# Kernel optimization log

Hardware: AMD Instinct MI355X
Metric: run time of the kernel (lower is better)

Reference implementation:

```python
import jax, jax.numpy as jnp
import numpy as np

N, E, H, C, NG = 50000, 800000, 4, 64, 32
HC = H * C  # 256


def setup_inputs() -> dict:
    key = jax.random.key(0)
    ks = jax.random.split(key, 32)
    f32 = jnp.float32
    def rn(k, shape, s=0.1):
        return jax.random.normal(k, shape, dtype=f32) * s
    inp = {}
    inp['x'] = jax.random.normal(ks[0], (N, 4), dtype=f32)
    inp['edge_index'] = jax.random.randint(ks[1], (2, E), 0, N, dtype=jnp.int32)
    inp['edge_attr'] = jax.random.normal(ks[2], (E, 1), dtype=f32)
    inp['batch'] = jnp.sort(jax.random.randint(ks[3], (N,), 0, NG, dtype=jnp.int32))
    # encoder
    inp['enc_w'] = rn(ks[4], (4, 64)); inp['enc_b'] = rn(ks[5], (64,))
    # GATv2 layer 1: in 64 -> H*C (lin_l source, lin_r target, lin_edge, att, bias)
    inp['g1_wl'] = rn(ks[6], (64, HC)); inp['g1_bl'] = rn(ks[7], (HC,))
    inp['g1_wr'] = rn(ks[8], (64, HC)); inp['g1_br'] = rn(ks[9], (HC,))
    inp['g1_we'] = rn(ks[10], (1, HC))
    inp['g1_att'] = rn(ks[11], (H, C))
    inp['g1_bias'] = rn(ks[12], (HC,))
    # GATv2 layer 2: in 256 -> H*C
    inp['g2_wl'] = rn(ks[13], (HC, HC)); inp['g2_bl'] = rn(ks[14], (HC,))
    inp['g2_wr'] = rn(ks[15], (HC, HC)); inp['g2_br'] = rn(ks[16], (HC,))
    inp['g2_we'] = rn(ks[17], (1, HC))
    inp['g2_att'] = rn(ks[18], (H, C))
    inp['g2_bias'] = rn(ks[19], (HC,))
    # post MLP: 256 -> 128 (LayerNorm, ReLU) -> 64 (ReLU)
    inp['p1_w'] = rn(ks[20], (HC, 128)); inp['p1_b'] = rn(ks[21], (128,))
    inp['ln_g'] = jnp.ones((128,), dtype=f32); inp['ln_b'] = jnp.zeros((128,), dtype=f32)
    inp['p2_w'] = rn(ks[22], (128, 64)); inp['p2_b'] = rn(ks[23], (64,))
    return inp


def _gatv2_layer(x, src, dst, eattr, wl, bl, wr, br, we, att, bias):
    # PyG GATv2Conv: alpha_e = att . leaky_relu(lin_l(x_src) + lin_r(x_dst) + lin_edge(e))
    n = x.shape[0]
    xl = (x @ wl + bl).reshape(n, H, C)   # source-side messages
    xr = (x @ wr + br).reshape(n, H, C)   # target-side
    e = (eattr @ we).reshape(-1, H, C)
    m = jax.nn.leaky_relu(xl[src] + xr[dst] + e, 0.2)        # [E',H,C]
    alpha = jnp.einsum('ehc,hc->eh', m, att)                  # [E',H]
    amax = jax.lax.stop_gradient(jax.ops.segment_max(alpha, dst, num_segments=n))
    ex = jnp.exp(alpha - amax[dst])
    den = jax.ops.segment_sum(ex, dst, num_segments=n)
    a = ex / den[dst]                                          # softmax per dst node
    out = jax.ops.segment_sum(a[:, :, None] * xl[src], dst, num_segments=n)
    return out.reshape(n, HC) + bias


def reference(x, edge_index, edge_attr, batch, enc_w, enc_b,
              g1_wl, g1_bl, g1_wr, g1_br, g1_we, g1_att, g1_bias,
              g2_wl, g2_bl, g2_wr, g2_br, g2_we, g2_att, g2_bias,
              p1_w, p1_b, ln_g, ln_b, p2_w, p2_b):
    n = x.shape[0]
    src0, dst0 = edge_index[0], edge_index[1]
    # PyG default add_self_loops=True with fill_value='mean' for edge_attr
    deg = jnp.maximum(jax.ops.segment_sum(jnp.ones_like(edge_attr[:, 0]), dst0, num_segments=n), 1.0)
    loop_attr = jax.ops.segment_sum(edge_attr, dst0, num_segments=n) / deg[:, None]
    idx = jnp.arange(n, dtype=src0.dtype)
    src = jnp.concatenate([src0, idx]); dst = jnp.concatenate([dst0, idx])
    eattr = jnp.concatenate([edge_attr, loop_attr], axis=0)
    h = jax.nn.relu(x @ enc_w + enc_b)
    h = jax.nn.relu(_gatv2_layer(h, src, dst, eattr, g1_wl, g1_bl, g1_wr, g1_br, g1_we, g1_att, g1_bias))
    h = jax.nn.relu(_gatv2_layer(h, src, dst, eattr, g2_wl, g2_bl, g2_wr, g2_br, g2_we, g2_att, g2_bias))
    # global mean pool over graphs
    cnt = jnp.maximum(jax.ops.segment_sum(jnp.ones((n,), h.dtype), batch, num_segments=NG), 1.0)
    g = jax.ops.segment_sum(h, batch, num_segments=NG) / cnt[:, None]
    # post MLP (dropout is identity in eval)
    z = g @ p1_w + p1_b
    mu = jnp.mean(z, axis=-1, keepdims=True)
    var = jnp.mean((z - mu) ** 2, axis=-1, keepdims=True)
    z = (z - mu) / jnp.sqrt(var + 1e-5) * ln_g + ln_b
    z = jax.nn.relu(z)
    z = jax.nn.relu(z @ p2_w + p2_b)
    return z
```

## Files before the change

### kernel.cpp

```cpp
#include <hip/hip_runtime.h>

#define CDIV(a,b) (((a)+(b)-1)/(b))

typedef __bf16 bf16_t;
typedef bf16_t bf16x8 __attribute__((ext_vector_type(8)));
typedef bf16_t bf16x4 __attribute__((ext_vector_type(4)));
typedef float floatx4 __attribute__((ext_vector_type(4)));
typedef float floatx2 __attribute__((ext_vector_type(2)));

__device__ __forceinline__ int sigma2(int p) {
    int tile = p >> 7, hh = (p >> 6) & 1, m = (p >> 2) & 15, c = p & 3;
    return tile * 128 + (hh * 4 + c) * 16 + m;
}

__device__ __forceinline__ floatx2 up2(unsigned v) {
    floatx2 r;
    r.x = __uint_as_float(v << 16);
    r.y = __uint_as_float(v & 0xffff0000u);
    return r;
}

__global__ void k_deg(const int* __restrict__ ei, const float* __restrict__ ea,
                      int* __restrict__ deg, float* __restrict__ lsum, int E) {
    int e = blockIdx.x * 256 + threadIdx.x;
    if (e >= E) return;
    int d = ei[E + e];
    atomicAdd(&deg[d], 1);
    atomicAdd(&lsum[d], ea[e]);
}

__global__ void k_scanA(const int* __restrict__ deg, int* __restrict__ part, int n) {
    __shared__ int sh[256];
    int t = threadIdx.x;
    int i = blockIdx.x * 256 + t;
    int v = (i < n) ? deg[i] + 1 : 0;
    sh[t] = v;
    __syncthreads();
    for (int d = 128; d > 0; d >>= 1) { if (t < d) sh[t] += sh[t + d]; __syncthreads(); }
    if (t == 0) part[blockIdx.x] = sh[0];
}
__global__ void k_scanB(int* __restrict__ part, int nb) {
    __shared__ int sh[256];
    int t = threadIdx.x;
    int v = (t < nb) ? part[t] : 0;
    sh[t] = v;
    __syncthreads();
    for (int d = 1; d < 256; d <<= 1) {
        int u = (t >= d) ? sh[t - d] : 0;
        __syncthreads();
        sh[t] += u;
        __syncthreads();
    }
    if (t < nb) part[t] = sh[t] - v;
}
__global__ void k_scanC(const int* __restrict__ deg, const int* __restrict__ part,
                        int* __restrict__ off, float* __restrict__ lsum, int n) {
    __shared__ int sh[256];
    int t = threadIdx.x;
    int i = blockIdx.x * 256 + t;
    int dv = (i < n) ? deg[i] : 0;
    int v = (i < n) ? dv + 1 : 0;
    sh[t] = v;
    __syncthreads();
    for (int d = 1; d < 256; d <<= 1) {
        int u = (t >= d) ? sh[t - d] : 0;
        __syncthreads();
        sh[t] += u;
        __syncthreads();
    }
    int excl = part[blockIdx.x] + sh[t] - v;
    if (i < n) {
        off[i] = excl;
        lsum[i] = lsum[i] / fmaxf((float)dv, 1.0f);
    }
    if (i == n - 1) off[n] = excl + v;
}

__global__ void k_fill(const int* __restrict__ ei, const float* __restrict__ ea,
                       const float* __restrict__ lattr, const int* __restrict__ off,
                       int* __restrict__ cursor, int2* __restrict__ csr, int E, int n) {
    int e = blockIdx.x * 256 + threadIdx.x;
    int EE = E + n;
    if (e >= EE) return;
    int s, d; float a;
    if (e < E) { s = ei[e]; d = ei[E + e]; a = ea[e]; }
    else       { s = e - E; d = s;         a = lattr[s]; }
    int pos = off[d] + atomicAdd(&cursor[d], 1);
    csr[pos] = make_int2(s, __float_as_int(a));
}

__global__ void k_wcast2(const float* __restrict__ Wl, const float* __restrict__ Wr,
                         const float* __restrict__ bl, const float* __restrict__ br,
                         bf16_t* __restrict__ Wt, float* __restrict__ bias2,
                         int K, int kshift, int permK,
                         const float* __restrict__ we, const float* __restrict__ att,
                         const float* __restrict__ cb,
                         float* __restrict__ wep, float* __restrict__ attp,
                         float* __restrict__ cbp) {
    int idx = blockIdx.x * 256 + threadIdx.x;
    if (idx < 512) bias2[idx] = (idx < 256) ? bl[idx] : br[idx - 256];
    if (idx < 256) {
        int sg = sigma2(idx);
        wep[idx] = we[sg]; attp[idx] = att[sg]; cbp[idx] = cb[sg];
    }
    if (idx >= 512 * K) return;
    int nn = idx >> kshift, k = idx & (K - 1);
    int ks = permK ? sigma2(k) : k;
    float v = (nn < 256) ? Wl[ks * 256 + nn] : Wr[ks * 256 + (nn - 256)];
    Wt[idx] = (bf16_t)v;
}

__global__ __launch_bounds__(256) void k_gemm1_fused(
        const float* __restrict__ x, const float* __restrict__ encw,
        const float* __restrict__ encb, const bf16_t* __restrict__ Wt,
        const float* __restrict__ bias2, bf16_t* __restrict__ XL,
        bf16_t* __restrict__ XR, int nrows) {
    __shared__ bf16_t As[128 * 32];
    __shared__ bf16_t Bs[128 * 32];
    int tid = threadIdx.x;
    int w = tid >> 6, lane = tid & 63;
    int quad = lane >> 4, m = lane & 15;
    int row0 = blockIdx.x * 128;
    int n0 = blockIdx.y * 128;
    floatx4 acc[2][8];
#pragma unroll
    for (int rt = 0; rt < 2; ++rt)
#pragma unroll
        for (int ct = 0; ct < 8; ++ct)
            acc[rt][ct] = (floatx4){0.f, 0.f, 0.f, 0.f};

    for (int k0 = 0; k0 < 64; k0 += 32) {
        __syncthreads();
#pragma unroll
        for (int i = 0; i < 2; ++i) {
            int c = tid + i * 256;
            int r = c >> 2, kc = c & 3;
            int sw = (kc + (r >> 1)) & 3;
            int gr = row0 + r; if (gr >= nrows) gr = nrows - 1;
            float4 xv = ((const float4*)x)[gr];
            bf16x8 v;
#pragma unroll
            for (int kk = 0; kk < 8; ++kk) {
                int k = k0 + kc * 8 + kk;
                float s = encb[k];
                s = fmaf(xv.x, encw[k], s);
                s = fmaf(xv.y, encw[64 + k], s);
                s = fmaf(xv.z, encw[128 + k], s);
                s = fmaf(xv.w, encw[192 + k], s);
                v[kk] = (bf16_t)fmaxf(s, 0.0f);
            }
            *(bf16x8*)&As[r * 32 + sw * 8] = v;
        }
#pragma unroll
        for (int i = 0; i < 2; ++i) {
            int c = tid + i * 256;
            int r = c >> 2, kc = c & 3;
            int sw = (kc + (r >> 1)) & 3;
            bf16x8 v = *(const bf16x8*)&Wt[(size_t)(n0 + r) * 64 + k0 + kc * 8];
            *(bf16x8*)&Bs[r * 32 + sw * 8] = v;
        }
        __syncthreads();
        bf16x8 af[2], bfr[8];
#pragma unroll
        for (int rt = 0; rt < 2; ++rt) {
            int ar = w * 32 + rt * 16 + m;
            af[rt] = *(bf16x8*)&As[ar * 32 + (((quad + (ar >> 1)) & 3) * 8)];
        }
#pragma unroll
        for (int ct = 0; ct < 8; ++ct) {
            int br = ct * 16 + m;
            bfr[ct] = *(bf16x8*)&Bs[br * 32 + (((quad + (br >> 1)) & 3) * 8)];
        }
#pragma unroll
        for (int ct = 0; ct < 8; ++ct) {
            acc[0][ct] = __builtin_amdgcn_mfma_f32_16x16x32_bf16(af[0], bfr[ct], acc[0][ct], 0, 0, 0);
            acc[1][ct] = __builtin_amdgcn_mfma_f32_16x16x32_bf16(af[1], bfr[ct], acc[1][ct], 0, 0, 0);
        }
    }
    int tile = (n0 >> 7) & 1;
    bf16_t* dst = (n0 < 256) ? XL : XR;
    float bv[8];
#pragma unroll
    for (int ct = 0; ct < 8; ++ct) bv[ct] = bias2[n0 + ct * 16 + m];
#pragma unroll
    for (int rt = 0; rt < 2; ++rt) {
#pragma unroll
        for (int i = 0; i < 4; ++i) {
            int row = row0 + w * 32 + rt * 16 + quad * 4 + i;
            if (row < nrows) {
                bf16x4 v0, v1;
#pragma unroll
                for (int ct = 0; ct < 4; ++ct) {
                    v0[ct] = (bf16_t)(acc[rt][ct][i] + bv[ct]);
                    v1[ct] = (bf16_t)(acc[rt][ct + 4][i] + bv[ct + 4]);
                }
                *(bf16x4*)&dst[(size_t)row * 256 + tile * 128 + m * 4] = v0;
                *(bf16x4*)&dst[(size_t)row * 256 + tile * 128 + 64 + m * 4] = v1;
            }
        }
    }
}

__global__ __launch_bounds__(256) void k_gemm_mfma(
        const bf16_t* __restrict__ Hb, const bf16_t* __restrict__ Wt,
        const float* __restrict__ bias2, bf16_t* __restrict__ XL,
        bf16_t* __restrict__ XR, int nrows, int K) {
    __shared__ bf16_t As[128 * 32];
    __shared__ bf16_t Bs[128 * 32];
    int tid = threadIdx.x;
    int w = tid >> 6, lane = tid & 63;
    int quad = lane >> 4, m = lane & 15;
    int row0 = blockIdx.x * 128;
    int n0 = blockIdx.y * 128;
    floatx4 acc[2][8];
#pragma unroll
    for (int rt = 0; rt < 2; ++rt)
#pragma unroll
        for (int ct = 0; ct < 8; ++ct)
            acc[rt][ct] = (floatx4){0.f, 0.f, 0.f, 0.f};

    for (int k0 = 0; k0 < K; k0 += 32) {
        __syncthreads();
#pragma unroll
        for (int i = 0; i < 2; ++i) {
            int c = tid + i * 256;
            int r = c >> 2, kc = c & 3;
            int sw = (kc + (r >> 1)) & 3;
            int gr = row0 + r; if (gr >= nrows) gr = nrows - 1;
            bf16x8 v = *(const bf16x8*)&Hb[(size_t)gr * K + k0 + kc * 8];
            *(bf16x8*)&As[r * 32 + sw * 8] = v;
        }
#pragma unroll
        for (int i = 0; i < 2; ++i) {
            int c = tid + i * 256;
            int r = c >> 2, kc = c & 3;
            int sw = (kc + (r >> 1)) & 3;
            bf16x8 v = *(const bf16x8*)&Wt[(size_t)(n0 + r) * K + k0 + kc * 8];
            *(bf16x8*)&Bs[r * 32 + sw * 8] = v;
        }
        __syncthreads();
        bf16x8 af[2], bfr[8];
#pragma unroll
        for (int rt = 0; rt < 2; ++rt) {
            int ar = w * 32 + rt * 16 + m;
            af[rt] = *(bf16x8*)&As[ar * 32 + (((quad + (ar >> 1)) & 3) * 8)];
        }
#pragma unroll
        for (int ct = 0; ct < 8; ++ct) {
            int br = ct * 16 + m;
            bfr[ct] = *(bf16x8*)&Bs[br * 32 + (((quad + (br >> 1)) & 3) * 8)];
        }
#pragma unroll
        for (int ct = 0; ct < 8; ++ct) {
            acc[0][ct] = __builtin_amdgcn_mfma_f32_16x16x32_bf16(af[0], bfr[ct], acc[0][ct], 0, 0, 0);
            acc[1][ct] = __builtin_amdgcn_mfma_f32_16x16x32_bf16(af[1], bfr[ct], acc[1][ct], 0, 0, 0);
        }
    }
    int tile = (n0 >> 7) & 1;
    bf16_t* dst = (n0 < 256) ? XL : XR;
    float bv[8];
#pragma unroll
    for (int ct = 0; ct < 8; ++ct) bv[ct] = bias2[n0 + ct * 16 + m];
#pragma unroll
    for (int rt = 0; rt < 2; ++rt) {
#pragma unroll
        for (int i = 0; i < 4; ++i) {
            int row = row0 + w * 32 + rt * 16 + quad * 4 + i;
            if (row < nrows) {
                bf16x4 v0, v1;
#pragma unroll
                for (int ct = 0; ct < 4; ++ct) {
                    v0[ct] = (bf16_t)(acc[rt][ct][i] + bv[ct]);
                    v1[ct] = (bf16_t)(acc[rt][ct + 4][i] + bv[ct + 4]);
                }
                *(bf16x4*)&dst[(size_t)row * 256 + tile * 128 + m * 4] = v0;
                *(bf16x4*)&dst[(size_t)row * 256 + tile * 128 + 64 + m * 4] = v1;
            }
        }
    }
}

__device__ __forceinline__ void pair_step(
        int p, int p1, int half, int loff,
        const int2* __restrict__ csr, const bf16_t* __restrict__ XL,
        floatx2 xr01, floatx2 xr23, floatx2 xr45, floatx2 xr67,
        floatx2 wv01, floatx2 wv23, floatx2 wv45, floatx2 wv67,
        floatx2 av01, floatx2 av23, floatx2 av45, floatx2 av67,
        float& s, floatx2& a01, floatx2& a23, floatx2& a45, floatx2& a67) {
    int idx = p + half;
    bool valid = idx < p1;
    int idc = valid ? idx : p1 - 1;
    int2 ed = csr[idc];
    int src = ed.x;
    float eav = __int_as_float(ed.y);
    uint4 u = *(const uint4*)((const char*)XL + (size_t)src * 512 + loff);
    floatx2 x01 = up2(u.x), x23 = up2(u.y), x45 = up2(u.z), x67 = up2(u.w);
    floatx2 t01 = x01 + xr01 + eav * wv01;
    floatx2 t23 = x23 + xr23 + eav * wv23;
    floatx2 t45 = x45 + xr45 + eav * wv45;
    floatx2 t67 = x67 + xr67 + eav * wv67;
    t01 = __builtin_elementwise_max(t01, 0.2f * t01);
    t23 = __builtin_elementwise_max(t23, 0.2f * t23);
    t45 = __builtin_elementwise_max(t45, 0.2f * t45);
    t67 = __builtin_elementwise_max(t67, 0.2f * t67);
    floatx2 d = t01 * av01 + t23 * av23 + t45 * av45 + t67 * av67;
    float al = d.x + d.y;
    al += __shfl_xor(al, 1);
    al += __shfl_xor(al, 2);
    al += __shfl_xor(al, 4);
    float wg = valid ? exp2f(al) : 0.0f;
    s += wg;
    a01 += wg * x01; a23 += wg * x23; a45 += wg * x45; a67 += wg * x67;
}

__global__ __launch_bounds__(256, 8) void k_conv(
                       const bf16_t* __restrict__ XL, const bf16_t* __restrict__ XR,
                       const float* __restrict__ wep, const float* __restrict__ attp,
                       const int2* __restrict__ csr,
                       const int* __restrict__ off, const float* __restrict__ cbp,
                       bf16_t* __restrict__ outb, int n) {
    int wid = (blockIdx.x * 256 + threadIdx.x) >> 6;
    int lane = threadIdx.x & 63;
    if (wid >= n) return;
    int l = lane & 31, half = lane >> 5;
    int loff = l * 16;
    uint4 ur = *(const uint4*)((const char*)XR + (size_t)wid * 512 + loff);
    floatx2 xr01 = up2(ur.x), xr23 = up2(ur.y), xr45 = up2(ur.z), xr67 = up2(ur.w);
    float4 wa = ((const float4*)wep)[2 * l], wb = ((const float4*)wep)[2 * l + 1];
    float4 aa = ((const float4*)attp)[2 * l], ab = ((const float4*)attp)[2 * l + 1];
    floatx2 wv01 = {wa.x, wa.y}, wv23 = {wa.z, wa.w};
    floatx2 wv45 = {wb.x, wb.y}, wv67 = {wb.z, wb.w};
    const float LOG2E = 1.44269504f;
    floatx2 av01 = {aa.x * LOG2E, aa.y * LOG2E}, av23 = {aa.z * LOG2E, aa.w * LOG2E};
    floatx2 av45 = {ab.x * LOG2E, ab.y * LOG2E}, av67 = {ab.z * LOG2E, ab.w * LOG2E};
    int p0 = off[wid], p1 = off[wid + 1];
    float s = 0.f;
    floatx2 a01 = {0.f, 0.f}, a23 = {0.f, 0.f}, a45 = {0.f, 0.f}, a67 = {0.f, 0.f};
    int p = p0;
    for (; p + 4 <= p1; p += 4) {
        pair_step(p,     p1, half, loff, csr, XL, xr01, xr23, xr45, xr67,
                  wv01, wv23, wv45, wv67, av01, av23, av45, av67, s, a01, a23, a45, a67);
        pair_step(p + 2, p1, half, loff, csr, XL, xr01, xr23, xr45, xr67,
                  wv01, wv23, wv45, wv67, av01, av23, av45, av67, s, a01, a23, a45, a67);
    }
    for (; p < p1; p += 2)
        pair_step(p,     p1, half, loff, csr, XL, xr01, xr23, xr45, xr67,
                  wv01, wv23, wv45, wv67, av01, av23, av45, av67, s, a01, a23, a45, a67);
    s += __shfl_xor(s, 32);
    a01.x += __shfl_xor(a01.x, 32); a01.y += __shfl_xor(a01.y, 32);
    a23.x += __shfl_xor(a23.x, 32); a23.y += __shfl_xor(a23.y, 32);
    a45.x += __shfl_xor(a45.x, 32); a45.y += __shfl_xor(a45.y, 32);
    a67.x += __shfl_xor(a67.x, 32); a67.y += __shfl_xor(a67.y, 32);
    if (half == 0) {
        float inv = 1.0f / s;
        float4 ba = ((const float4*)cbp)[2 * l], bb = ((const float4*)cbp)[2 * l + 1];
        bf16x8 ob;
        ob[0] = (bf16_t)fmaxf(fmaf(a01.x, inv, ba.x), 0.f);
        ob[1] = (bf16_t)fmaxf(fmaf(a01.y, inv, ba.y), 0.f);
        ob[2] = (bf16_t)fmaxf(fmaf(a23.x, inv, ba.z), 0.f);
        ob[3] = (bf16_t)fmaxf(fmaf(a23.y, inv, ba.w), 0.f);
        ob[4] = (bf16_t)fmaxf(fmaf(a45.x, inv, bb.x), 0.f);
        ob[5] = (bf16_t)fmaxf(fmaf(a45.y, inv, bb.y), 0.f);
        ob[6] = (bf16_t)fmaxf(fmaf(a67.x, inv, bb.z), 0.f);
        ob[7] = (bf16_t)fmaxf(fmaf(a67.y, inv, bb.w), 0.f);
        *(bf16x8*)&outb[(size_t)wid * 256 + l * 8] = ob;
    }
}

__global__ void k_pool(const bf16_t* __restrict__ h, const int* __restrict__ batch,
                       float* __restrict__ gsum, float* __restrict__ gcnt, int n) {
    int j = threadIdx.x;
    int start = blockIdx.x * 32;
    if (start >= n) return;
    int end = start + 32; if (end > n) end = n;
    int cur = batch[start];
    float acc = 0.0f, cnt = 0.0f;
    for (int i = start; i < end; ++i) {
        int g = batch[i];
        if (g != cur) {
            atomicAdd(&gsum[cur * 256 + j], acc);
            if (j == 0) atomicAdd(&gcnt[cur], cnt);
            acc = 0.0f; cnt = 0.0f; cur = g;
        }
        acc += (float)h[(size_t)i * 256 + j];
        cnt += 1.0f;
    }
    atomicAdd(&gsum[cur * 256 + j], acc);
    if (j == 0) atomicAdd(&gcnt[cur], cnt);
}

__global__ void k_mlp(const float* __restrict__ gsum, const float* __restrict__ gcnt,
                      const float* __restrict__ p1w, const float* __restrict__ p1b,
                      const float* __restrict__ lng, const float* __restrict__ lnb,
                      const float* __restrict__ p2w, const float* __restrict__ p2b,
                      float* __restrict__ out) {
    int g = blockIdx.x;
    int t = threadIdx.x;
    __shared__ float gv[256];
    __shared__ float z[128];
    __shared__ float red[128];
    float invc = 1.0f / fmaxf(gcnt[g], 1.0f);
    gv[sigma2(t)]       = gsum[g * 256 + t] * invc;
    gv[sigma2(t + 128)] = gsum[g * 256 + 128 + t] * invc;
    __syncthreads();
    float z1 = p1b[t];
    for (int k = 0; k < 256; ++k) z1 = fmaf(gv[k], p1w[k * 128 + t], z1);
    red[t] = z1;
    __syncthreads();
    for (int d = 64; d > 0; d >>= 1) { if (t < d) red[t] += red[t + d]; __syncthreads(); }
    float mu = red[0] * (1.0f / 128.0f);
    __syncthreads();
    float dz = z1 - mu;
    red[t] = dz * dz;
    __syncthreads();
    for (int d = 64; d > 0; d >>= 1) { if (t < d) red[t] += red[t + d]; __syncthreads(); }
    float var = red[0] * (1.0f / 128.0f);
    float zn = dz * rsqrtf(var + 1e-5f) * lng[t] + lnb[t];
    z[t] = fmaxf(zn, 0.0f);
    __syncthreads();
    if (t < 64) {
        float o = p2b[t];
        for (int k = 0; k < 128; ++k) o = fmaf(z[k], p2w[k * 64 + t], o);
        out[g * 64 + t] = fmaxf(o, 0.0f);
    }
}

extern "C" void kernel_launch(void* const* d_in, const int* in_sizes, int n_in,
                              void* d_out, int out_size, void* d_ws, size_t ws_size,
                              hipStream_t stream) {
    const float* x      = (const float*)d_in[0];
    const int*   ei     = (const int*)d_in[1];
    const float* ea     = (const float*)d_in[2];
    const int*   batch  = (const int*)d_in[3];
    const float* enc_w  = (const float*)d_in[4];
    const float* enc_b  = (const float*)d_in[5];
    const float* g1_wl  = (const float*)d_in[6];
    const float* g1_bl  = (const float*)d_in[7];
    const float* g1_wr  = (const float*)d_in[8];
    const float* g1_br  = (const float*)d_in[9];
    const float* g1_we  = (const float*)d_in[10];
    const float* g1_att = (const float*)d_in[11];
    const float* g1_bias= (const float*)d_in[12];
    const float* g2_wl  = (const float*)d_in[13];
    const float* g2_bl  = (const float*)d_in[14];
    const float* g2_wr  = (const float*)d_in[15];
    const float* g2_br  = (const float*)d_in[16];
    const float* g2_we  = (const float*)d_in[17];
    const float* g2_att = (const float*)d_in[18];
    const float* g2_bias= (const float*)d_in[19];
    const float* p1_w   = (const float*)d_in[20];
    const float* p1_b   = (const float*)d_in[21];
    const float* ln_g   = (const float*)d_in[22];
    const float* ln_b   = (const float*)d_in[23];
    const float* p2_w   = (const float*)d_in[24];
    const float* p2_b   = (const float*)d_in[25];
    float* out = (float*)d_out;

    const int N  = in_sizes[3];
    const int E  = in_sizes[1] / 2;
    const int EE = E + N;
    const int NB = CDIV(N, 256);

    bf16_t* XL  = (bf16_t*)d_ws;
    bf16_t* XR  = XL + (size_t)N * 256;
    bf16_t* Hb  = XR + (size_t)N * 256;
    bf16_t* Wt  = Hb + (size_t)N * 256;
    int2*  csr  = (int2*)(Wt + 512 * 256);
    float* lsum  = (float*)(csr + EE);
    float* gsum  = lsum + N;
    float* gcnt  = gsum + 32 * 256;
    int*   deg   = (int*)(gcnt + 32);
    int*   cursor= deg + N;
    float* bias2 = (float*)(cursor + N);
    float* wep   = bias2 + 512;
    float* attp  = wep + 256;
    float* cbp   = attp + 256;
    int*   part  = (int*)(cbp + 256);
    int*   off   = part + 256;

    hipMemsetAsync(lsum, 0, (size_t)(3 * N + 32 * 256 + 32) * sizeof(float), stream);

    k_deg<<<CDIV(E, 256), 256, 0, stream>>>(ei, ea, deg, lsum, E);
    k_scanA<<<NB, 256, 0, stream>>>(deg, part, N);
    k_scanB<<<1, 256, 0, stream>>>(part, NB);
    k_scanC<<<NB, 256, 0, stream>>>(deg, part, off, lsum, N);
    k_fill<<<CDIV(EE, 256), 256, 0, stream>>>(ei, ea, lsum, off, cursor, csr, E, N);

    dim3 ggrid(CDIV(N, 128), 4);

    k_wcast2<<<CDIV(512 * 64, 256), 256, 0, stream>>>(g1_wl, g1_wr, g1_bl, g1_br, Wt, bias2,
                                                      64, 6, 0, g1_we, g1_att, g1_bias,
                                                      wep, attp, cbp);
    k_gemm1_fused<<<ggrid, 256, 0, stream>>>(x, enc_w, enc_b, Wt, bias2, XL, XR, N);
    k_conv<<<CDIV(N, 4), 256, 0, stream>>>(XL, XR, wep, attp, csr, off, cbp, Hb, N);

    k_wcast2<<<CDIV(512 * 256, 256), 256, 0, stream>>>(g2_wl, g2_wr, g2_bl, g2_br, Wt, bias2,
                                                       256, 8, 1, g2_we, g2_att, g2_bias,
                                                       wep, attp, cbp);
    k_gemm_mfma<<<ggrid, 256, 0, stream>>>(Hb, Wt, bias2, XL, XR, N, 256);
    k_conv<<<CDIV(N, 4), 256, 0, stream>>>(XL, XR, wep, attp, csr, off, cbp, Hb, N);

    k_pool<<<CDIV(N, 32), 256, 0, stream>>>(Hb, batch, gsum, gcnt, N);
    k_mlp<<<32, 128, 0, stream>>>(gsum, gcnt, p1_w, p1_b, ln_g, ln_b, p2_w, p2_b, out);
}
```

Before: 502.5 us.

## Keep A-tile fragments in registers and loop over all output column tiles per block

Both GEMM kernels now launch one block per 128-row strip and loop over the four 128-column output tiles inside the block. A fragments are loaded from shared memory only on the first column tile and kept in registers, so the activation reads (and, for layer 1, the encoder computation) happen once per strip instead of four times. In exchange each block does four times the work, the grid shrinks to about 391 blocks, and register pressure rises (16 bf16x8 fragments in the second GEMM). The launch-bounds occupancy hint is also removed from the conv kernel.

```diff
diff --git a/kernel.cpp b/kernel.cpp
--- a/kernel.cpp
+++ b/kernel.cpp
@@ -121,160 +121,175 @@
     int w = tid >> 6, lane = tid & 63;
     int quad = lane >> 4, m = lane & 15;
     int row0 = blockIdx.x * 128;
-    int n0 = blockIdx.y * 128;
+    bf16x8 afr[2][2];
     floatx4 acc[2][8];
-#pragma unroll
-    for (int rt = 0; rt < 2; ++rt)
-#pragma unroll
-        for (int ct = 0; ct < 8; ++ct)
-            acc[rt][ct] = (floatx4){0.f, 0.f, 0.f, 0.f};
-
-    for (int k0 = 0; k0 < 64; k0 += 32) {
-        __syncthreads();
-#pragma unroll
-        for (int i = 0; i < 2; ++i) {
-            int c = tid + i * 256;
-            int r = c >> 2, kc = c & 3;
-            int sw = (kc + (r >> 1)) & 3;
-            int gr = row0 + r; if (gr >= nrows) gr = nrows - 1;
-            float4 xv = ((const float4*)x)[gr];
-            bf16x8 v;
-#pragma unroll
-            for (int kk = 0; kk < 8; ++kk) {
-                int k = k0 + kc * 8 + kk;
-                float s = encb[k];
-                s = fmaf(xv.x, encw[k], s);
-                s = fmaf(xv.y, encw[64 + k], s);
-                s = fmaf(xv.z, encw[128 + k], s);
-                s = fmaf(xv.w, encw[192 + k], s);
-                v[kk] = (bf16_t)fmaxf(s, 0.0f);
-            }
-            *(bf16x8*)&As[r * 32 + sw * 8] = v;
+
+    for (int ctile = 0; ctile < 4; ++ctile) {
+        int n0 = ctile * 128;
+#pragma unroll
+        for (int rt = 0; rt < 2; ++rt)
+#pragma unroll
+            for (int ct = 0; ct < 8; ++ct)
+                acc[rt][ct] = (floatx4){0.f, 0.f, 0.f, 0.f};
+        for (int k0c = 0; k0c < 2; ++k0c) {
+            __syncthreads();
+            if (ctile == 0) {
+#pragma unroll
+                for (int i = 0; i < 2; ++i) {
+                    int c = tid + i * 256;
+                    int r = c >> 2, kc = c & 3;
+                    int sw = (kc + (r >> 1)) & 3;
+                    int gr = row0 + r; if (gr >= nrows) gr = nrows - 1;
+                    float4 xv = ((const float4*)x)[gr];
+                    bf16x8 v;
+#pragma unroll
+                    for (int kk = 0; kk < 8; ++kk) {
+                        int k = k0c * 32 + kc * 8 + kk;
+                        float s = encb[k];
+                        s = fmaf(xv.x, encw[k], s);
+                        s = fmaf(xv.y, encw[64 + k], s);
+                        s = fmaf(xv.z, encw[128 + k], s);
+                        s = fmaf(xv.w, encw[192 + k], s);
+                        v[kk] = (bf16_t)fmaxf(s, 0.0f);
+                    }
+                    *(bf16x8*)&As[r * 32 + sw * 8] = v;
+                }
+            }
+#pragma unroll
+            for (int i = 0; i < 2; ++i) {
+                int c = tid + i * 256;
+                int r = c >> 2, kc = c & 3;
+                int sw = (kc + (r >> 1)) & 3;
+                bf16x8 v = *(const bf16x8*)&Wt[(size_t)(n0 + r) * 64 + k0c * 32 + kc * 8];
+                *(bf16x8*)&Bs[r * 32 + sw * 8] = v;
+            }
+            __syncthreads();
+            if (ctile == 0) {
+#pragma unroll
+                for (int rt = 0; rt < 2; ++rt) {
+                    int ar = w * 32 + rt * 16 + m;
+                    afr[k0c][rt] = *(bf16x8*)&As[ar * 32 + (((quad + (ar >> 1)) & 3) * 8)];
+                }
+            }
+            bf16x8 bfr[8];
+#pragma unroll
+            for (int ct = 0; ct < 8; ++ct) {
+                int br = ct * 16 + m;
+                bfr[ct] = *(bf16x8*)&Bs[br * 32 + (((quad + (br >> 1)) & 3) * 8)];
+            }
+#pragma unroll
+            for (int ct = 0; ct < 8; ++ct) {
+                acc[0][ct] = __builtin_amdgcn_mfma_f32_16x16x32_bf16(afr[k0c][0], bfr[ct], acc[0][ct], 0, 0, 0);
+                acc[1][ct] = __builtin_amdgcn_mfma_f32_16x16x32_bf16(afr[k0c][1], bfr[ct], acc[1][ct], 0, 0, 0);
+            }
         }
-#pragma unroll
-        for (int i = 0; i < 2; ++i) {
-            int c = tid + i * 256;
-            int r = c >> 2, kc = c & 3;
-            int sw = (kc + (r >> 1)) & 3;
-            bf16x8 v = *(const bf16x8*)&Wt[(size_t)(n0 + r) * 64 + k0 + kc * 8];
-            *(bf16x8*)&Bs[r * 32 + sw * 8] = v;
+        int tile = ctile & 1;
+        bf16_t* dst = (ctile < 2) ? XL : XR;
+        float bv[8];
+#pragma unroll
+        for (int ct = 0; ct < 8; ++ct) bv[ct] = bias2[n0 + ct * 16 + m];
+#pragma unroll
+        for (int rt = 0; rt < 2; ++rt) {
+#pragma unroll
+            for (int i = 0; i < 4; ++i) {
+                int row = row0 + w * 32 + rt * 16 + quad * 4 + i;
+                if (row < nrows) {
+                    bf16x4 v0, v1;
+#pragma unroll
+                    for (int ct = 0; ct < 4; ++ct) {
+                        v0[ct] = (bf16_t)(acc[rt][ct][i] + bv[ct]);
+                        v1[ct] = (bf16_t)(acc[rt][ct + 4][i] + bv[ct + 4]);
+                    }
+                    *(bf16x4*)&dst[(size_t)row * 256 + tile * 128 + m * 4] = v0;
+                    *(bf16x4*)&dst[(size_t)row * 256 + tile * 128 + 64 + m * 4] = v1;
+                }
+            }
         }
-        __syncthreads();
-        bf16x8 af[2], bfr[8];
-#pragma unroll
-        for (int rt = 0; rt < 2; ++rt) {
-            int ar = w * 32 + rt * 16 + m;
-            af[rt] = *(bf16x8*)&As[ar * 32 + (((quad + (ar >> 1)) & 3) * 8)];
-        }
-#pragma unroll
-        for (int ct = 0; ct < 8; ++ct) {
-            int br = ct * 16 + m;
-            bfr[ct] = *(bf16x8*)&Bs[br * 32 + (((quad + (br >> 1)) & 3) * 8)];
-        }
-#pragma unroll
-        for (int ct = 0; ct < 8; ++ct) {
-            acc[0][ct] = __builtin_amdgcn_mfma_f32_16x16x32_bf16(af[0], bfr[ct], acc[0][ct], 0, 0, 0);
-            acc[1][ct] = __builtin_amdgcn_mfma_f32_16x16x32_bf16(af[1], bfr[ct], acc[1][ct], 0, 0, 0);
-        }
-    }
-    int tile = (n0 >> 7) & 1;
-    bf16_t* dst = (n0 < 256) ? XL : XR;
-    float bv[8];
-#pragma unroll
-    for (int ct = 0; ct < 8; ++ct) bv[ct] = bias2[n0 + ct * 16 + m];
-#pragma unroll
-    for (int rt = 0; rt < 2; ++rt) {
-#pragma unroll
-        for (int i = 0; i < 4; ++i) {
-            int row = row0 + w * 32 + rt * 16 + quad * 4 + i;
-            if (row < nrows) {
-                bf16x4 v0, v1;
-#pragma unroll
-                for (int ct = 0; ct < 4; ++ct) {
-                    v0[ct] = (bf16_t)(acc[rt][ct][i] + bv[ct]);
-                    v1[ct] = (bf16_t)(acc[rt][ct + 4][i] + bv[ct + 4]);
-                }
-                *(bf16x4*)&dst[(size_t)row * 256 + tile * 128 + m * 4] = v0;
-                *(bf16x4*)&dst[(size_t)row * 256 + tile * 128 + 64 + m * 4] = v1;
-            }
-        }
-    }
-}
-
-__global__ __launch_bounds__(256) void k_gemm_mfma(
+    }
+}
+
+__global__ __launch_bounds__(256) void k_gemm2(
         const bf16_t* __restrict__ Hb, const bf16_t* __restrict__ Wt,
         const float* __restrict__ bias2, bf16_t* __restrict__ XL,
-        bf16_t* __restrict__ XR, int nrows, int K) {
+        bf16_t* __restrict__ XR, int nrows) {
+    const int K = 256;
     __shared__ bf16_t As[128 * 32];
     __shared__ bf16_t Bs[128 * 32];
     int tid = threadIdx.x;
     int w = tid >> 6, lane = tid & 63;
     int quad = lane >> 4, m = lane & 15;
     int row0 = blockIdx.x * 128;
-    int n0 = blockIdx.y * 128;
+    bf16x8 afr[8][2];
     floatx4 acc[2][8];
-#pragma unroll
-    for (int rt = 0; rt < 2; ++rt)
-#pragma unroll
-        for (int ct = 0; ct < 8; ++ct)
-            acc[rt][ct] = (floatx4){0.f, 0.f, 0.f, 0.f};
-
-    for (int k0 = 0; k0 < K; k0 += 32) {
-        __syncthreads();
-#pragma unroll
-        for (int i = 0; i < 2; ++i) {
-            int c = tid + i * 256;
-            int r = c >> 2, kc = c & 3;
-            int sw = (kc + (r >> 1)) & 3;
-            int gr = row0 + r; if (gr >= nrows) gr = nrows - 1;
-            bf16x8 v = *(const bf16x8*)&Hb[(size_t)gr * K + k0 + kc * 8];
-            *(bf16x8*)&As[r * 32 + sw * 8] = v;
+
+    for (int ctile = 0; ctile < 4; ++ctile) {
+        int n0 = ctile * 128;
+#pragma unroll
+        for (int rt = 0; rt < 2; ++rt)
+#pragma unroll
+            for (int ct = 0; ct < 8; ++ct)
+                acc[rt][ct] = (floatx4){0.f, 0.f, 0.f, 0.f};
+        for (int k0c = 0; k0c < 8; ++k0c) {
+            __syncthreads();
+            if (ctile == 0) {
+#pragma unroll
+                for (int i = 0; i < 2; ++i) {
+                    int c = tid + i * 256;
+                    int r = c >> 2, kc = c & 3;
+                    int sw = (kc + (r >> 1)) & 3;
+                    int gr = row0 + r; if (gr >= nrows) gr = nrows - 1;
+                    bf16x8 v = *(const bf16x8*)&Hb[(size_t)gr * K + k0c * 32 + kc * 8];
+                    *(bf16x8*)&As[r * 32 + sw * 8] = v;
+                }
+            }
+#pragma unroll
+            for (int i = 0; i < 2; ++i) {
+                int c = tid + i * 256;
+                int r = c >> 2, kc = c & 3;
+                int sw = (kc + (r >> 1)) & 3;
+                bf16x8 v = *(const bf16x8*)&Wt[(size_t)(n0 + r) * K + k0c * 32 + kc * 8];
+                *(bf16x8*)&Bs[r * 32 + sw * 8] = v;
+            }
+            __syncthreads();
+            if (ctile == 0) {
+#pragma unroll
+                for (int rt = 0; rt < 2; ++rt) {
+                    int ar = w * 32 + rt * 16 + m;
+                    afr[k0c][rt] = *(bf16x8*)&As[ar * 32 + (((quad + (ar >> 1)) & 3) * 8)];
+                }
+            }
+            bf16x8 bfr[8];
+#pragma unroll
+            for (int ct = 0; ct < 8; ++ct) {
+                int br = ct * 16 + m;
+                bfr[ct] = *(bf16x8*)&Bs[br * 32 + (((quad + (br >> 1)) & 3) * 8)];
+            }
+#pragma unroll
+            for (int ct = 0; ct < 8; ++ct) {
+                acc[0][ct] = __builtin_amdgcn_mfma_f32_16x16x32_bf16(afr[k0c][0], bfr[ct], acc[0][ct], 0, 0, 0);
+                acc[1][ct] = __builtin_amdgcn_mfma_f32_16x16x32_bf16(afr[k0c][1], bfr[ct], acc[1][ct], 0, 0, 0);
+            }
         }
-#pragma unroll
-        for (int i = 0; i < 2; ++i) {
-            int c = tid + i * 256;
-            int r = c >> 2, kc = c & 3;
-            int sw = (kc + (r >> 1)) & 3;
-            bf16x8 v = *(const bf16x8*)&Wt[(size_t)(n0 + r) * K + k0 + kc * 8];
-            *(bf16x8*)&Bs[r * 32 + sw * 8] = v;
-        }
-        __syncthreads();
-        bf16x8 af[2], bfr[8];
+        int tile = ctile & 1;
+        bf16_t* dst = (ctile < 2) ? XL : XR;
+        float bv[8];
+#pragma unroll
+        for (int ct = 0; ct < 8; ++ct) bv[ct] = bias2[n0 + ct * 16 + m];
 #pragma unroll
         for (int rt = 0; rt < 2; ++rt) {
-            int ar = w * 32 + rt * 16 + m;
-            af[rt] = *(bf16x8*)&As[ar * 32 + (((quad + (ar >> 1)) & 3) * 8)];
-        }
-#pragma unroll
-        for (int ct = 0; ct < 8; ++ct) {
-            int br = ct * 16 + m;
-            bfr[ct] = *(bf16x8*)&Bs[br * 32 + (((quad + (br >> 1)) & 3) * 8)];
-        }
-#pragma unroll
-        for (int ct = 0; ct < 8; ++ct) {
-            acc[0][ct] = __builtin_amdgcn_mfma_f32_16x16x32_bf16(af[0], bfr[ct], acc[0][ct], 0, 0, 0);
-            acc[1][ct] = __builtin_amdgcn_mfma_f32_16x16x32_bf16(af[1], bfr[ct], acc[1][ct], 0, 0, 0);
-        }
-    }
-    int tile = (n0 >> 7) & 1;
-    bf16_t* dst = (n0 < 256) ? XL : XR;
-    float bv[8];
-#pragma unroll
-    for (int ct = 0; ct < 8; ++ct) bv[ct] = bias2[n0 + ct * 16 + m];
-#pragma unroll
-    for (int rt = 0; rt < 2; ++rt) {
-#pragma unroll
-        for (int i = 0; i < 4; ++i) {
-            int row = row0 + w * 32 + rt * 16 + quad * 4 + i;
-            if (row < nrows) {
-                bf16x4 v0, v1;
-#pragma unroll
-                for (int ct = 0; ct < 4; ++ct) {
-                    v0[ct] = (bf16_t)(acc[rt][ct][i] + bv[ct]);
-                    v1[ct] = (bf16_t)(acc[rt][ct + 4][i] + bv[ct + 4]);
+#pragma unroll
+            for (int i = 0; i < 4; ++i) {
+                int row = row0 + w * 32 + rt * 16 + quad * 4 + i;
+                if (row < nrows) {
+                    bf16x4 v0, v1;
+#pragma unroll
+                    for (int ct = 0; ct < 4; ++ct) {
+                        v0[ct] = (bf16_t)(acc[rt][ct][i] + bv[ct]);
+                        v1[ct] = (bf16_t)(acc[rt][ct + 4][i] + bv[ct + 4]);
+                    }
+                    *(bf16x4*)&dst[(size_t)row * 256 + tile * 128 + m * 4] = v0;
+                    *(bf16x4*)&dst[(size_t)row * 256 + tile * 128 + 64 + m * 4] = v1;
                 }
-                *(bf16x4*)&dst[(size_t)row * 256 + tile * 128 + m * 4] = v0;
-                *(bf16x4*)&dst[(size_t)row * 256 + tile * 128 + 64 + m * 4] = v1;
             }
         }
     }
@@ -313,7 +328,7 @@
     a01 += wg * x01; a23 += wg * x23; a45 += wg * x45; a67 += wg * x67;
 }
 
-__global__ __launch_bounds__(256, 8) void k_conv(
+__global__ void k_conv(
                        const bf16_t* __restrict__ XL, const bf16_t* __restrict__ XR,
                        const float* __restrict__ wep, const float* __restrict__ attp,
                        const int2* __restrict__ csr,
@@ -486,18 +501,16 @@
     k_scanC<<<NB, 256, 0, stream>>>(deg, part, off, lsum, N);
     k_fill<<<CDIV(EE, 256), 256, 0, stream>>>(ei, ea, lsum, off, cursor, csr, E, N);
 
-    dim3 ggrid(CDIV(N, 128), 4);
-
     k_wcast2<<<CDIV(512 * 64, 256), 256, 0, stream>>>(g1_wl, g1_wr, g1_bl, g1_br, Wt, bias2,
                                                       64, 6, 0, g1_we, g1_att, g1_bias,
                                                       wep, attp, cbp);
-    k_gemm1_fused<<<ggrid, 256, 0, stream>>>(x, enc_w, enc_b, Wt, bias2, XL, XR, N);
+    k_gemm1_fused<<<CDIV(N, 128), 256, 0, stream>>>(x, enc_w, enc_b, Wt, bias2, XL, XR, N);
     k_conv<<<CDIV(N, 4), 256, 0, stream>>>(XL, XR, wep, attp, csr, off, cbp, Hb, N);
 
     k_wcast2<<<CDIV(512 * 256, 256), 256, 0, stream>>>(g2_wl, g2_wr, g2_bl, g2_br, Wt, bias2,
                                                        256, 8, 1, g2_we, g2_att, g2_bias,
                                                        wep, attp, cbp);
-    k_gemm_mfma<<<ggrid, 256, 0, stream>>>(Hb, Wt, bias2, XL, XR, N, 256);
+    k_gemm2<<<CDIV(N, 128), 256, 0, stream>>>(Hb, Wt, bias2, XL, XR, N);
     k_conv<<<CDIV(N, 4), 256, 0, stream>>>(XL, XR, wep, attp, csr, off, cbp, Hb, N);
 
     k_pool<<<CDIV(N, 32), 256, 0, stream>>>(Hb, batch, gsum, gcnt, N);
```

After: 474.5 us. 1.06x faster.
